# Performance work log

Hardware: AMD Instinct MI355X
Metric: run time of the kernel (lower is better)

## Reference

```python
import jax, jax.numpy as jnp
import numpy as np

EPS = 1e-5

def bn(x, gamma, beta):
    # BatchNorm1d training-mode stats over all dims except channel (last)
    axes = tuple(range(x.ndim - 1))
    m = jnp.mean(x, axis=axes)
    v = jnp.var(x, axis=axes)
    return (x - m) * jax.lax.rsqrt(v + EPS) * gamma + beta

def setup_inputs() -> dict:
    key = jax.random.key(0)
    ks = jax.random.split(key, 16)
    N, M, K = 16384, 65536, 16
    Cin, Csk, C, G = 256, 128, 256, 16
    s = 0.02
    w = lambda k, shape: jax.random.normal(k, shape, jnp.float32) * s
    z = lambda c: jnp.zeros((c,), jnp.float32)
    o = lambda c: jnp.ones((c,), jnp.float32)
    return {
        'coord': jax.random.uniform(ks[0], (N, 3), jnp.float32),
        'feat': jax.random.normal(ks[1], (N, Cin), jnp.float32),
        'skip_coord': jax.random.uniform(ks[2], (M, 3), jnp.float32),
        'skip_feat': jax.random.normal(ks[3], (M, Csk), jnp.float32),
        'cluster': jax.random.randint(ks[4], (M,), 0, N, jnp.int32),
        'reference_index': jax.random.randint(ks[5], (N, K), 0, N, jnp.int32),
        # proj (in->out) + BN
        'Wp': w(ks[6], (Cin, C)), 'bp': z(C), 'gp': o(C), 'bep': z(C),
        # proj_skip (skip->out) + BN
        'Ws': w(ks[7], (Csk, C)), 'bs': z(C), 'gs': o(C), 'bes': z(C),
        # key (out->out) + BN
        'Wk': w(ks[8], (C, C)), 'bk': z(C), 'gk': o(C), 'bek': z(C),
        # query (out->out) + BN
        'Wq': w(ks[9], (C, C)), 'bq': z(C), 'gq': o(C), 'beq': z(C),
        # linear_p_bias: Linear(3,out) BN ReLU Linear(out,out)
        'Wp1': w(ks[10], (3, C)), 'bp1': z(C), 'gp1': o(C), 'bep1': z(C),
        'Wp2': w(ks[11], (C, C)), 'bp2': z(C),
        # weight_encoding: Linear(out,g) BN ReLU Linear(g,g)
        'Ww1': w(ks[12], (C, G)), 'bw1': z(G), 'gw1': o(G), 'bew1': z(G),
        'Ww2': w(ks[13], (G, G)), 'bw2': z(G),
    }

def reference(coord, feat, skip_coord, skip_feat, cluster, reference_index,
              Wp, bp, gp, bep, Ws, bs, gs, bes, Wk, bk, gk, bek,
              Wq, bq, gq, beq, Wp1, bp1, gp1, bep1, Wp2, bp2,
              Ww1, bw1, gw1, bew1, Ww2, bw2):
    G = Ww2.shape[0]
    skip_p = jax.nn.relu(bn(skip_feat @ Ws + bs, gs, bes))      # [M, C]
    lres = jax.nn.relu(bn(feat @ Wp + bp, gp, bep))             # [N, C]
    hres = lres[cluster] + skip_p                                # [M, C]
    ref = reference_index[cluster]                               # [M, K]
    key = jax.nn.relu(bn(lres @ Wk + bk, gk, bek))              # [N, C]
    query = jax.nn.relu(bn(hres @ Wq + bq, gq, beq))            # [M, C]
    gkey = key[ref]                                              # [M, K, C]
    pos = coord[ref] - skip_coord[:, None, :]                    # [M, K, 3]
    value = lres[ref]                                            # [M, K, C]
    relation_qk = gkey - query[:, None, :]
    peb = jax.nn.relu(bn(pos @ Wp1 + bp1, gp1, bep1)) @ Wp2 + bp2
    relation_qk = relation_qk + peb
    value = value + peb
    weight = jax.nn.relu(bn(relation_qk @ Ww1 + bw1, gw1, bew1)) @ Ww2 + bw2  # [M,K,G]
    weight = jax.nn.softmax(weight, axis=1)
    mask = jnp.sign(ref + 1).astype(weight.dtype)                # [M, K]
    weight = weight * mask[:, :, None]
    Mn, Kn, C = value.shape
    value = value.reshape(Mn, Kn, G, C // G)
    out = jnp.einsum('nsgi,nsg->ngi', value, weight).reshape(Mn, C)
    return out + skip_p
```

## Files before the change

### kernel.cpp

```cpp
#include <hip/hip_runtime.h>


typedef unsigned short u16;
typedef unsigned int   u32;
typedef __attribute__((ext_vector_type(4))) float f32x4;
typedef __attribute__((ext_vector_type(8))) short s16x8;
typedef __attribute__((ext_vector_type(4))) int   i32x4;

#define NN 16384
#define MM 65536
#define MKCNT 1048576
#define EPS 1e-5f

__device__ __forceinline__ float uf(u16 u){ union{u32 i; float f;} x; x.i = ((u32)u)<<16; return x.f; }
__device__ __forceinline__ u16 fu(float f){ u32 x = __float_as_uint(f); u32 r = (x + 0x7fffu + ((x>>16)&1u))>>16; return (u16)r; }

__global__ void k_fill(float* o, int nsz){
  int i = blockIdx.x*256 + threadIdx.x;
  if(i < nsz) o[i] = 12345.0f;
}

__global__ __launch_bounds__(256) void k_count(const int* __restrict__ clu, int* __restrict__ cnt){
  int m = blockIdx.x*256 + threadIdx.x;
  atomicAdd(&cnt[clu[m]], 1);
}
__global__ __launch_bounds__(256) void k_scan(int* __restrict__ cnt, int* __restrict__ offs){
  __shared__ int part[256];
  int t = threadIdx.x;
  int s = 0;
  #pragma unroll 1
  for(int i=0;i<64;i++) s += cnt[t*64+i];
  part[t] = s;
  __syncthreads();
  if(t==0){ int run=0; for(int i=0;i<256;i++){ int tmp=part[i]; part[i]=run; run+=tmp; } }
  __syncthreads();
  int run = part[t];
  #pragma unroll 1
  for(int i=0;i<64;i++){ int c = cnt[t*64+i]; offs[t*64+i] = run; run += c; cnt[t*64+i] = 0; }
}
__global__ __launch_bounds__(256) void k_scatter(const int* __restrict__ clu, const int* __restrict__ offs,
                                                 int* __restrict__ cur, int* __restrict__ perm){
  int m = blockIdx.x*256 + threadIdx.x;
  int n = clu[m];
  int p = atomicAdd(&cur[n], 1);
  perm[offs[n] + p] = m;
}

__global__ __launch_bounds__(256) void k_prep(const float* __restrict__ Wp2, const float* __restrict__ Ww1,
                                              const float* __restrict__ bw1, const float* __restrict__ bp2,
                                              u16* __restrict__ W21T, float* __restrict__ c0){
  int t = blockIdx.x*256 + threadIdx.x;
  int c = t >> 4, j = t & 15;
  float a = 0.f;
  for(int c2=0;c2<256;c2++) a += Wp2[c*256+c2] * Ww1[c2*16+j];
  W21T[j*256 + c] = fu(a);
  if(t < 16){
    float s = bw1[t];
    for(int c2=0;c2<256;c2++) s += bp2[c2] * Ww1[c2*16+t];
    c0[t] = s;
  }
}

__global__ __launch_bounds__(256) void k_wp2t(const float* __restrict__ Wp2, u16* __restrict__ W2T){
  int i = blockIdx.x*256 + threadIdx.x;
  int col = i >> 8, cp = i & 255;
  W2T[col*256 + cp] = fu(Wp2[cp*256 + col]);
}

__global__ __launch_bounds__(256) void k_A(const float* __restrict__ coord, const float* __restrict__ Wp1,
                                           u16* __restrict__ A){
  int i = blockIdx.x*256 + threadIdx.x;
  int n = i >> 8, c = i & 255;
  float a = coord[n*3]*Wp1[c] + coord[n*3+1]*Wp1[256+c] + coord[n*3+2]*Wp1[512+c];
  A[i] = fu(a);
}

__device__ __forceinline__ void stage8(const float* p, u16* dst){
  f32x4 a = *(const f32x4*)p; f32x4 b = *(const f32x4*)(p+4);
  union { i32x4 v; u16 a[8]; } u;
  u.a[0]=fu(a[0]); u.a[1]=fu(a[1]); u.a[2]=fu(a[2]); u.a[3]=fu(a[3]);
  u.a[4]=fu(b[0]); u.a[5]=fu(b[1]); u.a[6]=fu(b[2]); u.a[7]=fu(b[3]);
  *(i32x4*)dst = u.v;
}
__device__ __forceinline__ void stage8(const u16* p, u16* dst){
  *(i32x4*)dst = *(const i32x4*)p;
}

template<typename AT, int KD>
__global__ __launch_bounds__(256) void k_gemm(const AT* __restrict__ Ag, const float* __restrict__ Bg,
                                              const float* __restrict__ bias, u16* __restrict__ Y,
                                              float* __restrict__ sSum, float* __restrict__ sSq)
{
  __shared__ __align__(16) u16 At[64][40];
  __shared__ __align__(16) u16 Bt[64][40];
  __shared__ float csum[64], csq[64];
  const int tid = threadIdx.x;
  const int lane = tid & 63, wv = tid >> 6;
  const int m0 = blockIdx.x * 64, n0 = blockIdx.y * 64;
  const int wr = (wv >> 1) * 32, wc = (wv & 1) * 32;
  const int fr = lane & 15, fq = lane >> 4, fk = fq * 8;
  f32x4 acc[2][2];
  acc[0][0]=acc[0][1]=acc[1][0]=acc[1][1]=(f32x4){0.f,0.f,0.f,0.f};
  const int arow = tid >> 2, akc = (tid & 3) * 8;
  const int brow = tid >> 3, bcol = (tid & 7) * 8;
  for(int k0 = 0; k0 < KD; k0 += 32){
    stage8(Ag + (size_t)(m0 + arow) * KD + k0 + akc, &At[arow][akc]);
    const float* bp = Bg + (size_t)(k0 + brow) * 256 + n0 + bcol;
    f32x4 b0 = *(const f32x4*)bp, b1 = *(const f32x4*)(bp+4);
    #pragma unroll
    for(int i=0;i<4;i++){ Bt[bcol + i][brow] = fu(b0[i]); Bt[bcol + 4 + i][brow] = fu(b1[i]); }
    __syncthreads();
    s16x8 af0 = *(const s16x8*)(&At[wr + fr][fk]);
    s16x8 af1 = *(const s16x8*)(&At[wr + 16 + fr][fk]);
    s16x8 bf0 = *(const s16x8*)(&Bt[wc + fr][fk]);
    s16x8 bf1 = *(const s16x8*)(&Bt[wc + 16 + fr][fk]);
    acc[0][0] = __builtin_amdgcn_mfma_f32_16x16x32_bf16(af0, bf0, acc[0][0], 0,0,0);
    acc[0][1] = __builtin_amdgcn_mfma_f32_16x16x32_bf16(af0, bf1, acc[0][1], 0,0,0);
    acc[1][0] = __builtin_amdgcn_mfma_f32_16x16x32_bf16(af1, bf0, acc[1][0], 0,0,0);
    acc[1][1] = __builtin_amdgcn_mfma_f32_16x16x32_bf16(af1, bf1, acc[1][1], 0,0,0);
    __syncthreads();
  }
  if(tid < 64){ csum[tid]=0.f; csq[tid]=0.f; }
  __syncthreads();
  #pragma unroll
  for(int ni=0; ni<2; ni++){
    const int lcol = wc + ni*16 + fr;
    const int col = n0 + lcol;
    const float bval = bias[col];
    float ps = 0.f, pq = 0.f;
    #pragma unroll
    for(int mi=0; mi<2; mi++){
      #pragma unroll
      for(int r=0; r<4; r++){
        const int row = m0 + wr + mi*16 + fq*4 + r;
        float v = acc[mi][ni][r] + bval;
        Y[(size_t)row*256 + col] = fu(v);
        ps += v; pq += v*v;
      }
    }
    atomicAdd(&csum[lcol], ps);
    atomicAdd(&csq[lcol], pq);
  }
  __syncthreads();
  if(tid < 64){
    atomicAdd(&sSum[n0 + tid], csum[tid]);
    atomicAdd(&sSq [n0 + tid], csq[tid]);
  }
}

__global__ void k_fin(const float* __restrict__ sum, const float* __restrict__ sq,
                      const float* __restrict__ gam, const float* __restrict__ bet,
                      float invn, int Cn, float* __restrict__ s, float* __restrict__ t){
  int c = threadIdx.x;
  if(c < Cn){
    float m = sum[c]*invn, v = sq[c]*invn - m*m;
    float sc = gam[c] * rsqrtf(v + EPS);
    s[c] = sc;
    t[c] = bet[c] - m*sc;
  }
}

__global__ __launch_bounds__(256) void k_lres(const u16* __restrict__ Y, const float* __restrict__ s,
                                              const float* __restrict__ t, u16* __restrict__ lres){
  int i8 = (blockIdx.x*256 + threadIdx.x)*8;
  int c0 = i8 & 255;
  union { i32x4 v; u16 a[8]; } yu, ou;
  yu.v = *(const i32x4*)(Y + i8);
  #pragma unroll
  for(int r=0;r<8;r++) ou.a[r] = fu(fmaxf(s[c0+r]*uf(yu.a[r]) + t[c0+r], 0.f));
  *(i32x4*)(lres + i8) = ou.v;
}

__global__ __launch_bounds__(256) void k_hres(const u16* __restrict__ Ys, const float* __restrict__ s,
                                              const float* __restrict__ t, const u16* __restrict__ lres,
                                              const int* __restrict__ cluster,
                                              u16* __restrict__ skipP, u16* __restrict__ hres){
  int i8 = (blockIdx.x*256 + threadIdx.x)*8;
  int m = i8 >> 8, c0 = i8 & 255;
  int n = cluster[m];
  union { i32x4 v; u16 a[8]; } yu, lu, su, hu;
  yu.v = *(const i32x4*)(Ys + i8);
  lu.v = *(const i32x4*)(lres + (size_t)n*256 + c0);
  #pragma unroll
  for(int r=0;r<8;r++){
    float v = fmaxf(s[c0+r]*uf(yu.a[r]) + t[c0+r], 0.f);
    su.a[r] = fu(v);
    hu.a[r] = fu(v + uf(lu.a[r]));
  }
  *(i32x4*)(skipP + i8) = su.v;
  *(i32x4*)(hres  + i8) = hu.v;
}

__global__ __launch_bounds__(256) void k_proj16(const u16* __restrict__ Y, const float* __restrict__ s,
                                                const float* __restrict__ t, const float* __restrict__ Ww1,
                                                float* __restrict__ Out, int rows){
  __shared__ float ss[256], tt[256];
  __shared__ float ww[256][17];
  for(int i = threadIdx.x; i < 256; i += 256){ ss[i]=s[i]; tt[i]=t[i]; }
  for(int i = threadIdx.x; i < 4096; i += 256) ww[i>>4][i&15] = Ww1[i];
  __syncthreads();
  int j = threadIdx.x & 15, rl = threadIdx.x >> 4;
  for(int r = blockIdx.x*16 + rl; r < rows; r += gridDim.x*16){
    float acc = 0.f;
    for(int c8 = 0; c8 < 32; c8++){
      union { i32x4 v; u16 a[8]; } yv;
      yv.v = *(const i32x4*)(Y + (size_t)r*256 + c8*8);
      #pragma unroll
      for(int e=0;e<8;e++){
        int c = c8*8 + e;
        float kv = fmaxf(ss[c]*uf(yv.a[e]) + tt[c], 0.f);
        acc += kv * ww[c][j];
      }
    }
    Out[(size_t)r*16 + j] = acc;
  }
}

__global__ __launch_bounds__(256) void k_bn1stats(const u16* __restrict__ A, const int* __restrict__ ri,
                                                  const int* __restrict__ clu, const float* __restrict__ skc,
                                                  const float* __restrict__ Wp1, const int* __restrict__ perm,
                                                  float* __restrict__ bs, float* __restrict__ bq){
  __shared__ int refs[4][16];
  __shared__ float scs[4][3];
  const int c = threadIdx.x;
  const float w0 = Wp1[c], w1 = Wp1[256+c], w2 = Wp1[512+c];
  float S=0.f, Q=0.f;
  const int i0 = blockIdx.x*64;
  for(int i = i0; i < i0+64; i += 4){
    if(c < 64){ int ml = c>>4, k = c&15; refs[ml][k] = ri[(size_t)clu[perm[i+ml]]*16 + k]; }
    else if(c < 80){ int q = c-64; int ml = q>>2, d = q&3;
      if(d < 3) scs[ml][d] = skc[(size_t)perm[i+ml]*3 + d]; }
    __syncthreads();
    #pragma unroll
    for(int ml=0; ml<4; ml++){
      float b = scs[ml][0]*w0 + scs[ml][1]*w1 + scs[ml][2]*w2;
      #pragma unroll
      for(int k=0;k<16;k++){
        float d = uf(A[(size_t)refs[ml][k]*256 + c]) - b;
        S += d; Q += d*d;
      }
    }
    __syncthreads();
  }
  atomicAdd(&bs[c], S);
  atomicAdd(&bq[c], Q);
}

__global__ __launch_bounds__(256) void k_S2h(const u16* __restrict__ A, const int* __restrict__ ri,
    const int* __restrict__ clu, const float* __restrict__ skc, const float* __restrict__ Wp1,
    const float* __restrict__ s1, const float* __restrict__ t1,
    const float* __restrict__ KW, const float* __restrict__ QW,
    const u16* __restrict__ W21T, const float* __restrict__ c0,
    const int* __restrict__ perm, u16* __restrict__ w1out, float* __restrict__ st)
{
  __shared__ int refs[4][16];
  __shared__ float scm[4][3];
  __shared__ __align__(16) u16 hb[4][16][264];
  __shared__ __align__(16) u16 w21t[16][264];
  __shared__ float r2s[16][17], r2q[16][17];
  const int tid = threadIdx.x, lane = tid & 63, wv = tid >> 6;
  for(int idx = tid; idx < 4096; idx += 256)
    w21t[idx>>8][idx&255] = W21T[idx];
  const int c = tid;
  const float w0 = Wp1[c], w1v = Wp1[256+c], w2v = Wp1[512+c];
  const float s1c = s1[c], t1c = t1[c];
  const int fj = lane & 15, fkb = (lane >> 4) * 8;
  const float c0j = c0[fj];
  __syncthreads();
  s16x8 bfr[8];
  #pragma unroll
  for(int s=0;s<8;s++) bfr[s] = *(const s16x8*)(&w21t[fj][fkb + 32*s]);
  float ls = 0.f, lq = 0.f;
  for(int ch = blockIdx.x; ch < MM/4; ch += gridDim.x){
    const int base = ch*4;
    if(tid < 64){ int ml = tid>>4, k = tid&15; refs[ml][k] = ri[(size_t)clu[perm[base+ml]]*16 + k]; }
    else if(tid < 80){ int q = tid-64; int ml = q>>2, d = q&3;
      if(d < 3) scm[ml][d] = skc[(size_t)perm[base+ml]*3 + d]; }
    __syncthreads();
    #pragma unroll
    for(int ml=0; ml<4; ml++){
      float b = scm[ml][0]*w0 + scm[ml][1]*w1v + scm[ml][2]*w2v;
      #pragma unroll
      for(int k=0;k<16;k++){
        float a = uf(A[(size_t)refs[ml][k]*256 + c]);
        hb[ml][k][c] = fu(fmaxf(s1c*(a-b)+t1c, 0.f));
      }
    }
    __syncthreads();
    {
      const int m = perm[base + wv];
      f32x4 acc = (f32x4){0.f,0.f,0.f,0.f};
      #pragma unroll
      for(int s=0;s<8;s++){
        s16x8 af = *(const s16x8*)(&hb[wv][fj][fkb + 32*s]);
        acc = __builtin_amdgcn_mfma_f32_16x16x32_bf16(af, bfr[s], acc, 0,0,0);
      }
      #pragma unroll
      for(int r=0;r<4;r++){
        int krow = (lane>>4)*4 + r;
        float v = acc[r] + c0j + KW[(size_t)refs[wv][krow]*16 + fj] - QW[(size_t)m*16 + fj];
        w1out[(size_t)m*256 + krow*16 + fj] = fu(v);
        ls += v; lq += v*v;
      }
    }
    __syncthreads();
  }
  {
    const int slot = wv*4 + (lane>>4);
    r2s[fj][slot] = ls;
    r2q[fj][slot] = lq;
    __syncthreads();
    if(tid < 16){
      float a=0.f, b=0.f;
      #pragma unroll
      for(int i=0;i<16;i++){ a += r2s[tid][i]; b += r2q[tid][i]; }
      atomicAdd(&st[tid], a);
      atomicAdd(&st[16+tid], b);
    }
  }
}

__global__ __launch_bounds__(256) void k_F1(const u16* __restrict__ w1, const float* __restrict__ s2,
    const float* __restrict__ t2, const float* __restrict__ Ww2, const float* __restrict__ bw2,
    u16* __restrict__ w2s)
{
  __shared__ float ul[16][16][17];
  const int tid = threadIdx.x;
  const int j = tid & 15, ml = tid >> 4;
  float ww2c[16];
  #pragma unroll
  for(int g=0; g<16; g++) ww2c[g] = Ww2[g*16+j];
  const float s2j = s2[j], t2j = t2[j], bw2j = bw2[j];
  for(int mg = blockIdx.x; mg < MM/16; mg += gridDim.x){
    size_t m = (size_t)mg*16 + ml;
    #pragma unroll
    for(int k=0;k<16;k++){
      float v = uf(w1[m*256 + k*16 + j]);
      ul[ml][k][j] = fmaxf(s2j*v + t2j, 0.f);
    }
    __syncthreads();
    float w2v[16];
    float mx = -1e30f;
    #pragma unroll
    for(int k=0;k<16;k++){
      float a = bw2j;
      #pragma unroll
      for(int g=0; g<16; g++) a += ul[ml][k][g]*ww2c[g];
      w2v[k] = a; mx = fmaxf(mx, a);
    }
    float den = 0.f;
    #pragma unroll
    for(int k=0;k<16;k++){ w2v[k] = __expf(w2v[k]-mx); den += w2v[k]; }
    float inv = 1.f/den;
    #pragma unroll
    for(int k=0;k<16;k++) w2s[m*256 + k*16 + j] = fu(w2v[k]*inv);
    __syncthreads();
  }
}

__global__ __launch_bounds__(256) void k_F2t(const u16* __restrict__ A, const int* __restrict__ ri,
    const int* __restrict__ clu, const float* __restrict__ skc, const float* __restrict__ Wp1,
    const float* __restrict__ s1, const float* __restrict__ t1,
    const u16* __restrict__ w2s, const u16* __restrict__ W2T, const float* __restrict__ bp2,
    const u16* __restrict__ lres, const u16* __restrict__ skipP, const int* __restrict__ perm,
    float* __restrict__ outp)
{
  __shared__ int mm[8];
  __shared__ int refs[8][16];
  __shared__ float scm[8][3];
  __shared__ float Sg[8][16];
  __shared__ __align__(16) u16 w2kT[8][16][40];
  __shared__ __align__(16) u16 hkc[8][32][40];
  __shared__ __align__(16) u16 Tb[8][17][40];
  const int tid = threadIdx.x, lane = tid & 63, wv = tid >> 6;
  for(int idx = tid; idx < 8*16; idx += 256){
    int ml = idx>>4, g = idx&15;
    #pragma unroll
    for(int k=16;k<32;k++) w2kT[ml][g][k] = 0;
  }
  for(int idx = tid; idx < 8*32; idx += 256){
    int ml = idx>>5, cp = idx&31;
    #pragma unroll
    for(int k=16;k<32;k++) hkc[ml][cp][k] = 0;
  }
  for(int sb = 0; sb < 4; sb++){
    const int base = (blockIdx.x*4 + sb)*8;
    if(tid < 8) mm[tid] = perm[base + tid];
    __syncthreads();
    if(tid < 128){ int ml = tid>>4, k = tid&15; refs[ml][k] = ri[(size_t)clu[mm[ml]]*16 + k]; }
    else if(tid < 160){ int q = tid-128; int ml = q>>2, d = q&3; if(d<3) scm[ml][d] = skc[(size_t)mm[ml]*3 + d]; }
    for(int idx = tid; idx < 2048; idx += 256){
      int ml = idx>>8, r = idx&255;
      int k = r>>4, g = r&15;
      w2kT[ml][g][k] = w2s[(size_t)mm[ml]*256 + r];
    }
    __syncthreads();
    if(tid < 128){
      int ml = tid>>4, g = tid&15;
      float s=0.f;
      #pragma unroll
      for(int k=0;k<16;k++) s += uf(w2kT[ml][g][k]);
      Sg[ml][g] = s;
    }
    f32x4 accG[4];
    #pragma unroll
    for(int gi=0; gi<4; gi++) accG[gi] = (f32x4){0.f,0.f,0.f,0.f};
    for(int q=0; q<8; q++){
      {
        const int cl = tid & 31, mlh = tid >> 5;
        const int cg = q*32 + cl;
        const float w0 = Wp1[cg], w1v = Wp1[256+cg], w2v = Wp1[512+cg];
        const float s1c = s1[cg], t1c = t1[cg];
        const float b = scm[mlh][0]*w0 + scm[mlh][1]*w1v + scm[mlh][2]*w2v;
        union { i32x4 v[2]; u16 a[16]; } hr;
        #pragma unroll
        for(int k=0;k<16;k++){
          float a = uf(A[(size_t)refs[mlh][k]*256 + cg]);
          hr.a[k] = fu(fmaxf(s1c*(a-b)+t1c, 0.f));
        }
        *(i32x4*)(&hkc[mlh][cl][0]) = hr.v[0];
        *(i32x4*)(&hkc[mlh][cl][8]) = hr.v[1];
      }
      __syncthreads();
      #pragma unroll
      for(int mq=0; mq<2; mq++){
        const int ml = wv*2 + mq;
        #pragma unroll
        for(int ct=0; ct<2; ct++){
          s16x8 af = *(const s16x8*)(&w2kT[ml][lane & 15][(lane>>4)*8]);
          s16x8 bf = *(const s16x8*)(&hkc[ml][ct*16 + (lane & 15)][(lane>>4)*8]);
          f32x4 d = __builtin_amdgcn_mfma_f32_16x16x32_bf16(af, bf, (f32x4){0.f,0.f,0.f,0.f}, 0,0,0);
          #pragma unroll
          for(int r=0;r<4;r++){
            int g = (lane>>4)*4 + r;
            Tb[ml][g][ct*16 + (lane & 15)] = fu(d[r]);
          }
        }
      }
      __syncthreads();
      #pragma unroll
      for(int gi=0; gi<4; gi++){
        const int g = wv*4 + gi;
        s16x8 tf = (s16x8){0,0,0,0,0,0,0,0};
        if((lane & 15) < 8)
          tf = *(const s16x8*)(&Tb[lane & 15][g][(lane>>4)*8]);
        s16x8 pf = *(const s16x8*)(&W2T[(size_t)(g*16 + (lane & 15))*256 + q*32 + (lane>>4)*8]);
        accG[gi] = __builtin_amdgcn_mfma_f32_16x16x32_bf16(tf, pf, accG[gi], 0,0,0);
      }
      __syncthreads();
    }
    float* opeb = (float*)&Tb[0][0][0];
    #pragma unroll
    for(int gi=0; gi<4; gi++){
      const int g = wv*4 + gi;
      #pragma unroll
      for(int r=0;r<4;r++){
        int ml = (lane>>4)*4 + r;
        if(ml < 8) opeb[ml*260 + g*16 + (lane & 15)] = accG[gi][r];
      }
    }
    __syncthreads();
    {
      const int cc = tid, g = cc>>4;
      const float bp2c = bp2[cc];
      for(int ml=0; ml<8; ml++){
        union { s16x8 v; u16 a[8]; } wr0, wr1;
        wr0.v = *(const s16x8*)(&w2kT[ml][g][0]);
        wr1.v = *(const s16x8*)(&w2kT[ml][g][8]);
        float ol0 = 0.f, ol1 = 0.f;
        #pragma unroll
        for(int k=0;k<8;k++){
          ol0 += uf(wr0.a[k])*uf(lres[(size_t)refs[ml][k]*256 + cc]);
          ol1 += uf(wr1.a[k])*uf(lres[(size_t)refs[ml][k+8]*256 + cc]);
        }
        size_t m = (size_t)mm[ml];
        outp[m*256 + cc] = opeb[ml*260 + cc] + Sg[ml][g]*bp2c + (ol0 + ol1) + uf(skipP[m*256 + cc]);
      }
    }
    __syncthreads();
  }
}

extern "C" void kernel_launch(void* const* d_in, const int* in_sizes, int n_in,
                              void* d_out, int out_size, void* d_ws, size_t ws_size,
                              hipStream_t stream){
  (void)in_sizes; (void)n_in;
  const float *coord=(const float*)d_in[0], *feat=(const float*)d_in[1];
  const float *skc=(const float*)d_in[2],   *skf=(const float*)d_in[3];
  const int *clu=(const int*)d_in[4],   *ri=(const int*)d_in[5];
  const float *Wp=(const float*)d_in[6],  *bp=(const float*)d_in[7],  *gp=(const float*)d_in[8],  *bep=(const float*)d_in[9];
  const float *Wsk=(const float*)d_in[10],*bs=(const float*)d_in[11], *gs=(const float*)d_in[12], *bes=(const float*)d_in[13];
  const float *Wk=(const float*)d_in[14], *bk=(const float*)d_in[15], *gk=(const float*)d_in[16], *bek=(const float*)d_in[17];
  const float *Wq=(const float*)d_in[18], *bq=(const float*)d_in[19], *gq=(const float*)d_in[20], *beq=(const float*)d_in[21];
  const float *Wp1=(const float*)d_in[22],                           *gp1=(const float*)d_in[24], *bep1=(const float*)d_in[25];
  const float *Wp2=(const float*)d_in[26], *bp2=(const float*)d_in[27];
  const float *Ww1=(const float*)d_in[28], *bw1=(const float*)d_in[29], *gw1=(const float*)d_in[30], *bew1=(const float*)d_in[31];
  const float *Ww2=(const float*)d_in[32], *bw2=(const float*)d_in[33];

  constexpr size_t OFF_A    = 0;
  constexpr size_t OFF_LRES = 8388608;
  constexpr size_t OFF_NY   = 16777216;
  constexpr size_t OFF_SKP  = 25165824;
  constexpr size_t OFF_M1   = 58720256;
  constexpr size_t OFF_M2   = 92274688;
  constexpr size_t OFF_KW   = 125829120;
  constexpr size_t OFF_QW   = 126877696;
  constexpr size_t OFF_ACC  = 131072000;
  constexpr size_t OFF_PAR  = 131084288;
  constexpr size_t OFF_W2T  = 131117056;
  constexpr size_t NEED     = 131248128;

  if(ws_size < NEED){
    k_fill<<<65536, 256, 0, stream>>>((float*)d_out, out_size);
    return;
  }
  char* ws = (char*)d_ws;
  u16* Ab    = (u16*)(ws + OFF_A);
  u16* lresb = (u16*)(ws + OFF_LRES);
  u16* nY    = (u16*)(ws + OFF_NY);
  u16* skipP = (u16*)(ws + OFF_SKP);
  u16* M1    = (u16*)(ws + OFF_M1);
  u16* M2    = (u16*)(ws + OFF_M2);
  float* KWp = (float*)(ws + OFF_KW);
  float* QWp = (float*)(ws + OFF_QW);
  u16* W2Tp  = (u16*)(ws + OFF_W2T);
  int* cntp  = (int*)(ws + OFF_NY);
  int* offsp = (int*)(ws + OFF_NY + 65536);
  int* permp = (int*)(ws + OFF_NY + 131072);
  float* ACC = (float*)(ws + OFF_ACC);
  float *gs0 = ACC+0,    *gq0 = ACC+256;
  float *gs1 = ACC+512,  *gq1 = ACC+768;
  float *gs2 = ACC+1024, *gq2 = ACC+1280;
  float *gs3 = ACC+1536, *gq3 = ACC+1792;
  float *b1s = ACC+2048, *b1q = ACC+2304;
  float *b2s = ACC+2560;
  float* PAR = (float*)(ws + OFF_PAR);
  float *sB0 = PAR+0,    *tB0 = PAR+256;
  float *sB1 = PAR+512,  *tB1 = PAR+768;
  float *sB2 = PAR+1024, *tB2 = PAR+1280;
  float *sB3 = PAR+1536, *tB3 = PAR+1792;
  float *s1p = PAR+2048, *t1p = PAR+2304;
  float *s2p = PAR+2560, *t2p = PAR+2576;
  float *c0p = PAR+2592;
  u16  *W21Tp= (u16*)(PAR+2608);

  hipMemsetAsync(ws + OFF_ACC, 0, 12288, stream);

  k_prep<<<16, 256, 0, stream>>>(Wp2, Ww1, bw1, bp2, W21Tp, c0p);
  k_wp2t<<<256, 256, 0, stream>>>(Wp2, W2Tp);
  k_A<<<16384, 256, 0, stream>>>(coord, Wp1, Ab);

  k_gemm<float,256><<<dim3(256,4), 256, 0, stream>>>(feat, Wp, bp, nY, gs0, gq0);
  k_fin<<<1, 256, 0, stream>>>(gs0, gq0, gp, bep, 1.f/(float)NN, 256, sB0, tB0);
  k_lres<<<2048, 256, 0, stream>>>(nY, sB0, tB0, lresb);

  k_gemm<float,128><<<dim3(1024,4), 256, 0, stream>>>(skf, Wsk, bs, M1, gs1, gq1);
  k_fin<<<1, 256, 0, stream>>>(gs1, gq1, gs, bes, 1.f/(float)MM, 256, sB1, tB1);
  k_hres<<<8192, 256, 0, stream>>>(M1, sB1, tB1, lresb, clu, skipP, M2);

  k_gemm<u16,256><<<dim3(256,4), 256, 0, stream>>>(lresb, Wk, bk, nY, gs2, gq2);
  k_fin<<<1, 256, 0, stream>>>(gs2, gq2, gk, bek, 1.f/(float)NN, 256, sB2, tB2);
  k_proj16<<<1024, 256, 0, stream>>>(nY, sB2, tB2, Ww1, KWp, NN);

  hipMemsetAsync(cntp, 0, 65536, stream);
  k_count<<<256, 256, 0, stream>>>(clu, cntp);
  k_scan<<<1, 256, 0, stream>>>(cntp, offsp);
  k_scatter<<<256, 256, 0, stream>>>(clu, offsp, cntp, permp);

  k_gemm<u16,256><<<dim3(1024,4), 256, 0, stream>>>(M2, Wq, bq, M1, gs3, gq3);
  k_fin<<<1, 256, 0, stream>>>(gs3, gq3, gq, beq, 1.f/(float)MM, 256, sB3, tB3);
  k_proj16<<<2048, 256, 0, stream>>>(M1, sB3, tB3, Ww1, QWp, MM);

  k_bn1stats<<<1024, 256, 0, stream>>>(Ab, ri, clu, skc, Wp1, permp, b1s, b1q);
  k_fin<<<1, 256, 0, stream>>>(b1s, b1q, gp1, bep1, 1.f/(float)MKCNT, 256, s1p, t1p);

  k_S2h<<<2048, 256, 0, stream>>>(Ab, ri, clu, skc, Wp1, s1p, t1p, KWp, QWp, W21Tp, c0p, permp, M1, b2s);
  k_fin<<<1, 256, 0, stream>>>(b2s, b2s+16, gw1, bew1, 1.f/(float)MKCNT, 16, s2p, t2p);

  k_F1<<<2048, 256, 0, stream>>>(M1, s2p, t2p, Ww2, bw2, M2);

  k_F2t<<<2048, 256, 0, stream>>>(Ab, ri, clu, skc, Wp1, s1p, t1p, M2, W2Tp, bp2, lresb, skipP, permp, (float*)d_out);
}
```

Before: 911.5 us.

## Prefold BN scale/shift into gathered position table and vectorize gathers

A new kernel applies the BN1 affine (s1*A+t1) to the per-point table A once, rewriting it as bf16 in place. The per-sample bias then reduces to s1*(skip_coord·Wp1), which is precomputed in shared memory for each gathered sample. k_S2h is also restructured so that each thread gathers contiguous 64-channel row segments with 16-byte vector loads, instead of one channel per thread. Doing this adds an extra pass over A and an additional bf16 rounding of the scaled values, while cutting per-element arithmetic and the number of scattered load instructions in the two gather-heavy kernels.

New measurement: 911.8 us. Within noise of the previous version (+0.0%).

```diff
diff --git a/kernel.cpp b/kernel.cpp
--- a/kernel.cpp
+++ b/kernel.cpp
@@ -73,6 +73,17 @@
   int n = i >> 8, c = i & 255;
   float a = coord[n*3]*Wp1[c] + coord[n*3+1]*Wp1[256+c] + coord[n*3+2]*Wp1[512+c];
   A[i] = fu(a);
+}
+
+__global__ __launch_bounds__(256) void k_Astar(u16* __restrict__ A, const float* __restrict__ s1,
+                                               const float* __restrict__ t1){
+  int i8 = (blockIdx.x*256 + threadIdx.x)*8;
+  int c0 = i8 & 255;
+  union { i32x4 v; u16 a[8]; } u, o;
+  u.v = *(const i32x4*)(A + i8);
+  #pragma unroll
+  for(int r=0;r<8;r++) o.a[r] = fu(s1[c0+r]*uf(u.a[r]) + t1[c0+r]);
+  *(i32x4*)(A + i8) = o.v;
 }
 
 __device__ __forceinline__ void stage8(const float* p, u16* dst){
@@ -246,9 +257,9 @@
   atomicAdd(&bq[c], Q);
 }
 
-__global__ __launch_bounds__(256) void k_S2h(const u16* __restrict__ A, const int* __restrict__ ri,
+__global__ __launch_bounds__(256) void k_S2h(const u16* __restrict__ As, const int* __restrict__ ri,
     const int* __restrict__ clu, const float* __restrict__ skc, const float* __restrict__ Wp1,
-    const float* __restrict__ s1, const float* __restrict__ t1,
+    const float* __restrict__ s1,
     const float* __restrict__ KW, const float* __restrict__ QW,
     const u16* __restrict__ W21T, const float* __restrict__ c0,
     const int* __restrict__ perm, u16* __restrict__ w1out, float* __restrict__ st)
@@ -257,15 +268,17 @@
   __shared__ float scm[4][3];
   __shared__ __align__(16) u16 hb[4][16][264];
   __shared__ __align__(16) u16 w21t[16][264];
+  __shared__ __align__(16) float bs2[4][260];
   __shared__ float r2s[16][17], r2q[16][17];
   const int tid = threadIdx.x, lane = tid & 63, wv = tid >> 6;
   for(int idx = tid; idx < 4096; idx += 256)
     w21t[idx>>8][idx&255] = W21T[idx];
   const int c = tid;
   const float w0 = Wp1[c], w1v = Wp1[256+c], w2v = Wp1[512+c];
-  const float s1c = s1[c], t1c = t1[c];
+  const float s1c = s1[c];
   const int fj = lane & 15, fkb = (lane >> 4) * 8;
   const float c0j = c0[fj];
+  const int ml4 = tid >> 6, kk = (tid >> 2) & 15, cp = tid & 3;
   __syncthreads();
   s16x8 bfr[8];
   #pragma unroll
@@ -278,12 +291,28 @@
       if(d < 3) scm[ml][d] = skc[(size_t)perm[base+ml]*3 + d]; }
     __syncthreads();
     #pragma unroll
-    for(int ml=0; ml<4; ml++){
-      float b = scm[ml][0]*w0 + scm[ml][1]*w1v + scm[ml][2]*w2v;
-      #pragma unroll
-      for(int k=0;k<16;k++){
-        float a = uf(A[(size_t)refs[ml][k]*256 + c]);
-        hb[ml][k][c] = fu(fmaxf(s1c*(a-b)+t1c, 0.f));
+    for(int ml=0; ml<4; ml++)
+      bs2[ml][c] = s1c*(scm[ml][0]*w0 + scm[ml][1]*w1v + scm[ml][2]*w2v);
+    __syncthreads();
+    {
+      const u16* arow = As + (size_t)refs[ml4][kk]*256 + cp*64;
+      u16* hrow = &hb[ml4][kk][cp*64];
+      const float* brow = &bs2[ml4][cp*64];
+      #pragma unroll
+      for(int b8=0;b8<8;b8++){
+        union { i32x4 v; u16 a[8]; } av, hv;
+        av.v = *(const i32x4*)(arow + b8*8);
+        f32x4 b0 = *(const f32x4*)(brow + b8*8);
+        f32x4 b1 = *(const f32x4*)(brow + b8*8 + 4);
+        hv.a[0] = fu(fmaxf(uf(av.a[0]) - b0[0], 0.f));
+        hv.a[1] = fu(fmaxf(uf(av.a[1]) - b0[1], 0.f));
+        hv.a[2] = fu(fmaxf(uf(av.a[2]) - b0[2], 0.f));
+        hv.a[3] = fu(fmaxf(uf(av.a[3]) - b0[3], 0.f));
+        hv.a[4] = fu(fmaxf(uf(av.a[4]) - b1[0], 0.f));
+        hv.a[5] = fu(fmaxf(uf(av.a[5]) - b1[1], 0.f));
+        hv.a[6] = fu(fmaxf(uf(av.a[6]) - b1[2], 0.f));
+        hv.a[7] = fu(fmaxf(uf(av.a[7]) - b1[3], 0.f));
+        *(i32x4*)(hrow + b8*8) = hv.v;
       }
     }
     __syncthreads();
@@ -358,9 +387,9 @@
   }
 }
 
-__global__ __launch_bounds__(256) void k_F2t(const u16* __restrict__ A, const int* __restrict__ ri,
+__global__ __launch_bounds__(256) void k_F2t(const u16* __restrict__ As, const int* __restrict__ ri,
     const int* __restrict__ clu, const float* __restrict__ skc, const float* __restrict__ Wp1,
-    const float* __restrict__ s1, const float* __restrict__ t1,
+    const float* __restrict__ s1,
     const u16* __restrict__ w2s, const u16* __restrict__ W2T, const float* __restrict__ bp2,
     const u16* __restrict__ lres, const u16* __restrict__ skipP, const int* __restrict__ perm,
     float* __restrict__ outp)
@@ -369,10 +398,13 @@
   __shared__ int refs[8][16];
   __shared__ float scm[8][3];
   __shared__ float Sg[8][16];
+  __shared__ float bs2F[8][260];
   __shared__ __align__(16) u16 w2kT[8][16][40];
   __shared__ __align__(16) u16 hkc[8][32][40];
   __shared__ __align__(16) u16 Tb[8][17][40];
   const int tid = threadIdx.x, lane = tid & 63, wv = tid >> 6;
+  const float w0 = Wp1[tid], w1g = Wp1[256+tid], w2g = Wp1[512+tid];
+  const float s1c = s1[tid];
   for(int idx = tid; idx < 8*16; idx += 256){
     int ml = idx>>4, g = idx&15;
     #pragma unroll
@@ -402,21 +434,23 @@
       for(int k=0;k<16;k++) s += uf(w2kT[ml][g][k]);
       Sg[ml][g] = s;
     }
+    #pragma unroll
+    for(int ml=0; ml<8; ml++)
+      bs2F[ml][tid] = s1c*(scm[ml][0]*w0 + scm[ml][1]*w1g + scm[ml][2]*w2g);
     f32x4 accG[4];
     #pragma unroll
     for(int gi=0; gi<4; gi++) accG[gi] = (f32x4){0.f,0.f,0.f,0.f};
+    __syncthreads();
     for(int q=0; q<8; q++){
       {
         const int cl = tid & 31, mlh = tid >> 5;
         const int cg = q*32 + cl;
-        const float w0 = Wp1[cg], w1v = Wp1[256+cg], w2v = Wp1[512+cg];
-        const float s1c = s1[cg], t1c = t1[cg];
-        const float b = scm[mlh][0]*w0 + scm[mlh][1]*w1v + scm[mlh][2]*w2v;
+        const float bsv = bs2F[mlh][cg];
         union { i32x4 v[2]; u16 a[16]; } hr;
         #pragma unroll
         for(int k=0;k<16;k++){
-          float a = uf(A[(size_t)refs[mlh][k]*256 + cg]);
-          hr.a[k] = fu(fmaxf(s1c*(a-b)+t1c, 0.f));
+          float a = uf(As[(size_t)refs[mlh][k]*256 + cg]);
+          hr.a[k] = fu(fmaxf(a - bsv, 0.f));
         }
         *(i32x4*)(&hkc[mlh][cl][0]) = hr.v[0];
         *(i32x4*)(&hkc[mlh][cl][8]) = hr.v[1];
@@ -573,11 +607,12 @@
 
   k_bn1stats<<<1024, 256, 0, stream>>>(Ab, ri, clu, skc, Wp1, permp, b1s, b1q);
   k_fin<<<1, 256, 0, stream>>>(b1s, b1q, gp1, bep1, 1.f/(float)MKCNT, 256, s1p, t1p);
-
-  k_S2h<<<2048, 256, 0, stream>>>(Ab, ri, clu, skc, Wp1, s1p, t1p, KWp, QWp, W21Tp, c0p, permp, M1, b2s);
+  k_Astar<<<2048, 256, 0, stream>>>(Ab, s1p, t1p);
+
+  k_S2h<<<2048, 256, 0, stream>>>(Ab, ri, clu, skc, Wp1, s1p, KWp, QWp, W21Tp, c0p, permp, M1, b2s);
   k_fin<<<1, 256, 0, stream>>>(b2s, b2s+16, gw1, bew1, 1.f/(float)MKCNT, 16, s2p, t2p);
 
   k_F1<<<2048, 256, 0, stream>>>(M1, s2p, t2p, Ww2, bw2, M2);
 
-  k_F2t<<<2048, 256, 0, stream>>>(Ab, ri, clu, skc, Wp1, s1p, t1p, M2, W2Tp, bp2, lresb, skipP, permp, (float*)d_out);
-}
+  k_F2t<<<2048, 256, 0, stream>>>(Ab, ri, clu, skc, Wp1, s1p, M2, W2Tp, bp2, lresb, skipP, permp, (float*)d_out);
+}
```
